# Optimization experiments

Measured on AMD Instinct MI355X. Metric: run time of the kernel, lower is better.

The kernel has to match this reference:

```python
import jax, jax.numpy as jnp
import numpy as np
from jax import lax

BS, T, D = 32, 2048, 256
H, L = 256, 2

def setup_inputs() -> dict:
    key = jax.random.key(0)
    ks = jax.random.split(key, 5)
    s = 1.0 / np.sqrt(H)
    x = jax.random.normal(ks[0], (BS, T, D), dtype=jnp.float32)
    Wx = jax.random.uniform(ks[1], (L, 3 * H, D), jnp.float32, -s, s)
    Wh = jax.random.uniform(ks[2], (L, 3 * H, H), jnp.float32, -s, s)
    bx = jax.random.uniform(ks[3], (L, 3 * H), jnp.float32, -s, s)
    bh = jax.random.uniform(ks[4], (L, 3 * H), jnp.float32, -s, s)
    return {"x": x, "Wx": Wx, "Wh": Wh, "bx": bx, "bh": bh}

def _gru_scan(gx, Wh, bh, h0):
    # gx: (T, bs, L, 3H) precomputed input-side gates; h0: (bs, L, H)
    def step(h, gx_t):
        gh = jnp.einsum('blh,lgh->blg', h, Wh) + bh  # (bs, L, 3H)
        xr, xz, xn = jnp.split(gx_t, 3, axis=-1)
        hr, hz, hn = jnp.split(gh, 3, axis=-1)
        r = jax.nn.sigmoid(xr + hr)
        z = jax.nn.sigmoid(xz + hz)
        n = jnp.tanh(xn + r * hn)
        h_new = (1.0 - z) * n + z * h
        return h_new, h_new
    _, hs = lax.scan(step, h0, gx)  # (T, bs, L, H)
    return hs

def reference(x, Wx, Wh, bx, bh):
    bs, t, _ = x.shape
    l, h = Wh.shape[0], Wh.shape[2]
    # Input-side gate projections for all timesteps/layers at once (each layer
    # consumes the raw input x_t, as in the source module).
    gx = jnp.einsum('btd,lgd->tblg', x, Wx) + bx  # (T, bs, L, 3H)
    h0 = jnp.zeros((bs, l, h), x.dtype)
    fwd = _gru_scan(gx, Wh, bh, h0)               # (T, bs, L, H)
    bwd = _gru_scan(gx[::-1], Wh, bh, h0)[::-1]   # reversed-time pass, same weights
    out = jnp.concatenate([fwd, bwd], axis=-1)    # (T, bs, L, 2H)
    # ordering matches source: for t in range(T): for layer in range(L)
    out = out.transpose(1, 0, 2, 3).reshape(bs, t * l, 2 * h)
    return out
```

## Files before the change

### kernel.cpp

```cpp
#include <hip/hip_runtime.h>


typedef _Float16 half8 __attribute__((ext_vector_type(8)));
typedef _Float16 half2_t __attribute__((ext_vector_type(2)));
typedef float floatx4 __attribute__((ext_vector_type(4)));

__device__ __forceinline__ float sigmoidf_fast(float x) {
    return 1.0f / (1.0f + __expf(-x));
}

__device__ __forceinline__ float tanh_fast(float x) {
    float ax = fabsf(x);
    float e = __expf(-2.0f * ax);
    float t = (1.0f - e) / (1.0f + e);
    return copysignf(t, x);
}

__global__ __launch_bounds__(256) void gemm_gx_kernel(
    const float* __restrict__ x,
    const float* __restrict__ Wx,
    const float* __restrict__ bx,
    _Float16* __restrict__ gx)
{
    __shared__ __align__(16) char lds[32768];
    _Float16* As = (_Float16*)lds;
    _Float16* Bs = (_Float16*)(lds + 8192);

    const int tid = threadIdx.x;
    const int m0 = blockIdx.x * 128;
    const int n0 = blockIdx.y * 128;
    const int wave = tid >> 6;
    const int lane = tid & 63;
    const int wm = wave & 1;
    const int wn = wave >> 1;
    const int frag = lane & 15;
    const int kg = lane >> 4;

    floatx4 acc[4][4];
#pragma unroll
    for (int a = 0; a < 4; ++a)
#pragma unroll
        for (int b = 0; b < 4; ++b)
            acc[a][b] = (floatx4){0.f, 0.f, 0.f, 0.f};

    for (int k0 = 0; k0 < 256; k0 += 32) {
        __syncthreads();
#pragma unroll
        for (int rep = 0; rep < 2; ++rep) {
            int idx = tid + rep * 256;
            int row = idx >> 2;
            int kc = idx & 3;
            const float4* ap = (const float4*)(x + (size_t)(m0 + row) * 256 + k0 + kc * 8);
            const float4* bp = (const float4*)(Wx + (size_t)(n0 + row) * 256 + k0 + kc * 8);
            float4 a0 = ap[0], a1 = ap[1];
            float4 b0 = bp[0], b1 = bp[1];
            half8 av = {(_Float16)a0.x, (_Float16)a0.y, (_Float16)a0.z, (_Float16)a0.w,
                        (_Float16)a1.x, (_Float16)a1.y, (_Float16)a1.z, (_Float16)a1.w};
            half8 bv = {(_Float16)b0.x, (_Float16)b0.y, (_Float16)b0.z, (_Float16)b0.w,
                        (_Float16)b1.x, (_Float16)b1.y, (_Float16)b1.z, (_Float16)b1.w};
            *(half8*)(As + (kc * 128 + row) * 8) = av;
            *(half8*)(Bs + (kc * 128 + row) * 8) = bv;
        }
        __syncthreads();

        half8 af[4], bfr[4];
#pragma unroll
        for (int tm = 0; tm < 4; ++tm)
            af[tm] = *(const half8*)(As + (kg * 128 + wm * 64 + tm * 16 + frag) * 8);
#pragma unroll
        for (int tn = 0; tn < 4; ++tn)
            bfr[tn] = *(const half8*)(Bs + (kg * 128 + wn * 64 + tn * 16 + frag) * 8);
#pragma unroll
        for (int tm = 0; tm < 4; ++tm)
#pragma unroll
            for (int tn = 0; tn < 4; ++tn)
                acc[tm][tn] = __builtin_amdgcn_mfma_f32_16x16x32_f16(
                    af[tm], bfr[tn], acc[tm][tn], 0, 0, 0);
    }

    __syncthreads();
    _Float16* epi = (_Float16*)lds;
#pragma unroll
    for (int tm = 0; tm < 4; ++tm) {
#pragma unroll
        for (int tn = 0; tn < 4; ++tn) {
            int col = wn * 64 + tn * 16 + frag;
            float bias = bx[n0 + col];
#pragma unroll
            for (int r = 0; r < 4; ++r) {
                int rowc = wm * 64 + tm * 16 + kg * 4 + r;
                epi[rowc * 128 + col] = (_Float16)(acc[tm][tn][r] + bias);
            }
        }
    }
    __syncthreads();

    int row = tid >> 1;
    int hs = tid & 1;
    int gm = m0 + row;
    int bb = gm >> 11;
    int tt = gm & 2047;
    int l = n0 / 768;
    int g0 = n0 - l * 768 + hs * 64;
    size_t oidx = (((size_t)bb * 2 + l) * 2048 + tt) * 768 + g0;
    const uint4* s = (const uint4*)(epi + row * 128 + hs * 64);
    uint4* d = (uint4*)(gx + oidx);
#pragma unroll
    for (int j = 0; j < 8; ++j) d[j] = s[j];
}

__global__ __launch_bounds__(512, 1) void gru_scan_kernel(
    const float* __restrict__ Wh,
    const float* __restrict__ bh,
    const _Float16* __restrict__ gx,
    float* __restrict__ out)
{
    const int c = blockIdx.x;
    const int b = c & 31;
    const int l = (c >> 5) & 1;
    const int dir = c >> 6;
    const int tid = threadIdx.x;
    const int i = tid & 255;
    const int q = tid >> 8;

    __shared__ __align__(16) _Float16 h2[256];
    __shared__ float part[3][256];
    __shared__ unsigned int gxb[2][384];

    half2_t wr[64], wz[64], wn_[64];
    {
        const float2* pr = (const float2*)(Wh + ((size_t)l * 768 + i) * 256 + q * 128);
        const float2* pz = (const float2*)(Wh + ((size_t)l * 768 + 256 + i) * 256 + q * 128);
        const float2* pn = (const float2*)(Wh + ((size_t)l * 768 + 512 + i) * 256 + q * 128);
#pragma unroll
        for (int j = 0; j < 64; ++j) {
            float2 a = pr[j], bb2 = pz[j], cc = pn[j];
            wr[j]  = (half2_t){(_Float16)a.x, (_Float16)a.y};
            wz[j]  = (half2_t){(_Float16)bb2.x, (_Float16)bb2.y};
            wn_[j] = (half2_t){(_Float16)cc.x, (_Float16)cc.y};
        }
    }

    const float bhr = bh[l * 768 + i];
    const float bhz = bh[l * 768 + 256 + i];
    const float bhn = bh[l * 768 + 512 + i];

    const unsigned int* gxrow = (const unsigned int*)gx + (size_t)(b * 2 + l) * 2048 * 384;
    float* outp = out + (size_t)b * 2048 * 1024 + (size_t)l * 512 + dir * 256 + i;

    if (tid < 256) h2[tid] = (_Float16)0.f;
    {
        int t0 = dir ? 2047 : 0;
        if (tid < 384) gxb[0][tid] = gxrow[(size_t)t0 * 384 + tid];
    }
    __syncthreads();

    float hreg = 0.f;

    for (int s = 0; s < 2048; ++s) {
        const int t = dir ? (2047 - s) : s;
        const int sn = (s < 2047) ? (s + 1) : s;
        const int tn = dir ? (2047 - sn) : sn;

        unsigned int pf = 0;
        if (tid < 384) pf = gxrow[(size_t)tn * 384 + tid];

        float ar = 0.f, az = 0.f, an = 0.f;
        const half2_t* hp = ((const half2_t*)h2) + q * 64;
#pragma unroll
        for (int j = 0; j < 64; ++j) {
            half2_t hv = hp[j];
            ar = __builtin_amdgcn_fdot2(wr[j], hv, ar, false);
            az = __builtin_amdgcn_fdot2(wz[j], hv, az, false);
            an = __builtin_amdgcn_fdot2(wn_[j], hv, an, false);
        }
        if (q) { part[0][i] = ar; part[1][i] = az; part[2][i] = an; }
        __syncthreads();

        if (tid < 256) {
            float ghr = ar + part[0][i] + bhr;
            float ghz = az + part[1][i] + bhz;
            float ghn = an + part[2][i] + bhn;
            const _Float16* gxc = (const _Float16*)(&gxb[s & 1][0]);
            float xr = (float)gxc[i];
            float xz = (float)gxc[256 + i];
            float xn = (float)gxc[512 + i];
            float r = sigmoidf_fast(xr + ghr);
            float z = sigmoidf_fast(xz + ghz);
            float n = tanh_fast(xn + r * ghn);
            float hnew = (1.f - z) * n + z * hreg;
            hreg = hnew;
            outp[(size_t)t * 1024] = hnew;
            h2[i] = (_Float16)hnew;
        }
        if (tid < 384) gxb[sn & 1][tid] = pf;
        __syncthreads();
    }
}

extern "C" void kernel_launch(void* const* d_in, const int* in_sizes, int n_in,
                              void* d_out, int out_size, void* d_ws, size_t ws_size,
                              hipStream_t stream) {
    const float* x  = (const float*)d_in[0];
    const float* Wx = (const float*)d_in[1];
    const float* Wh = (const float*)d_in[2];
    const float* bx = (const float*)d_in[3];
    const float* bh = (const float*)d_in[4];
    float* out = (float*)d_out;
    _Float16* gxbuf = (_Float16*)d_ws;

    gemm_gx_kernel<<<dim3(512, 12), 256, 0, stream>>>(x, Wx, bx, gxbuf);

    gru_scan_kernel<<<dim3(128), 512, 0, stream>>>(Wh, bh, gxbuf, out);
}
```

Measured before the change: 2.965 ms.

## Reduce GRU scan partial sums within waves via shuffles, double-buffer hidden state

Each output unit now has its two K-halves in the two halves of the same wave, so the partial sums combine with a cross-lane shuffle instead of a shared-memory array. This removes one of the two block barriers per timestep. The hidden state in shared memory is double-buffered, and the input-gate values are prefetched per thread straight from global memory into registers rather than staged through LDS. h is read with 128-bit LDS loads. A dead tanh computation is left in the code and should be optimized away; the waves_per_eu hint may change register allocation for the large register-resident weights.

```diff
diff --git a/kernel.cpp b/kernel.cpp
--- a/kernel.cpp
+++ b/kernel.cpp
@@ -109,7 +109,9 @@
     for (int j = 0; j < 8; ++j) d[j] = s[j];
 }
 
-__global__ __launch_bounds__(512, 1) void gru_scan_kernel(
+__global__ __launch_bounds__(512)
+__attribute__((amdgpu_waves_per_eu(2, 2)))
+void gru_scan_kernel(
     const float* __restrict__ Wh,
     const float* __restrict__ bh,
     const _Float16* __restrict__ gx,
@@ -120,12 +122,12 @@
     const int l = (c >> 5) & 1;
     const int dir = c >> 6;
     const int tid = threadIdx.x;
-    const int i = tid & 255;
-    const int q = tid >> 8;
-
-    __shared__ __align__(16) _Float16 h2[256];
-    __shared__ float part[3][256];
-    __shared__ unsigned int gxb[2][384];
+    const int wave = tid >> 6;
+    const int lane = tid & 63;
+    const int q = lane >> 5;
+    const int i = wave * 32 + (lane & 31);
+
+    __shared__ __align__(16) _Float16 h2[2][256];
 
     half2_t wr[64], wz[64], wn_[64];
     {
@@ -145,14 +147,15 @@
     const float bhz = bh[l * 768 + 256 + i];
     const float bhn = bh[l * 768 + 512 + i];
 
-    const unsigned int* gxrow = (const unsigned int*)gx + (size_t)(b * 2 + l) * 2048 * 384;
+    const _Float16* gxp = gx + (size_t)(b * 2 + l) * 2048 * 768;
     float* outp = out + (size_t)b * 2048 * 1024 + (size_t)l * 512 + dir * 256 + i;
 
-    if (tid < 256) h2[tid] = (_Float16)0.f;
-    {
-        int t0 = dir ? 2047 : 0;
-        if (tid < 384) gxb[0][tid] = gxrow[(size_t)t0 * 384 + tid];
-    }
+    if (tid < 256) h2[0][tid] = (_Float16)0.f;
+
+    const int t0 = dir ? 2047 : 0;
+    _Float16 cxr = gxp[(size_t)t0 * 768 + i];
+    _Float16 cxz = gxp[(size_t)t0 * 768 + 256 + i];
+    _Float16 cxn = gxp[(size_t)t0 * 768 + 512 + i];
     __syncthreads();
 
     float hreg = 0.f;
@@ -162,38 +165,51 @@
         const int sn = (s < 2047) ? (s + 1) : s;
         const int tn = dir ? (2047 - sn) : sn;
 
-        unsigned int pf = 0;
-        if (tid < 384) pf = gxrow[(size_t)tn * 384 + tid];
+        _Float16 pxr = gxp[(size_t)tn * 768 + i];
+        _Float16 pxz = gxp[(size_t)tn * 768 + 256 + i];
+        _Float16 pxn = gxp[(size_t)tn * 768 + 512 + i];
 
         float ar = 0.f, az = 0.f, an = 0.f;
-        const half2_t* hp = ((const half2_t*)h2) + q * 64;
-#pragma unroll
-        for (int j = 0; j < 64; ++j) {
-            half2_t hv = hp[j];
-            ar = __builtin_amdgcn_fdot2(wr[j], hv, ar, false);
-            az = __builtin_amdgcn_fdot2(wz[j], hv, az, false);
-            an = __builtin_amdgcn_fdot2(wn_[j], hv, an, false);
-        }
-        if (q) { part[0][i] = ar; part[1][i] = az; part[2][i] = an; }
-        __syncthreads();
-
-        if (tid < 256) {
-            float ghr = ar + part[0][i] + bhr;
-            float ghz = az + part[1][i] + bhz;
-            float ghn = an + part[2][i] + bhn;
-            const _Float16* gxc = (const _Float16*)(&gxb[s & 1][0]);
-            float xr = (float)gxc[i];
-            float xz = (float)gxc[256 + i];
-            float xn = (float)gxc[512 + i];
-            float r = sigmoidf_fast(xr + ghr);
-            float z = sigmoidf_fast(xz + ghz);
-            float n = tanh_fast(xn + r * ghn);
-            float hnew = (1.f - z) * n + z * hreg;
-            hreg = hnew;
+        const uint4* hbase = (const uint4*)(&h2[s & 1][0]) + (q << 4);
+#pragma unroll
+        for (int j = 0; j < 16; ++j) {
+            uint4 hv = hbase[j];
+            half2_t h0 = __builtin_bit_cast(half2_t, hv.x);
+            half2_t h1 = __builtin_bit_cast(half2_t, hv.y);
+            half2_t hg = __builtin_bit_cast(half2_t, hv.z);
+            half2_t h3 = __builtin_bit_cast(half2_t, hv.w);
+            ar = __builtin_amdgcn_fdot2(wr[4 * j + 0], h0, ar, false);
+            az = __builtin_amdgcn_fdot2(wz[4 * j + 0], h0, az, false);
+            an = __builtin_amdgcn_fdot2(wn_[4 * j + 0], h0, an, false);
+            ar = __builtin_amdgcn_fdot2(wr[4 * j + 1], h1, ar, false);
+            az = __builtin_amdgcn_fdot2(wz[4 * j + 1], h1, az, false);
+            an = __builtin_amdgcn_fdot2(wn_[4 * j + 1], h1, an, false);
+            ar = __builtin_amdgcn_fdot2(wr[4 * j + 2], hg, ar, false);
+            az = __builtin_amdgcn_fdot2(wz[4 * j + 2], hg, az, false);
+            an = __builtin_amdgcn_fdot2(wn_[4 * j + 2], hg, an, false);
+            ar = __builtin_amdgcn_fdot2(wr[4 * j + 3], h3, ar, false);
+            az = __builtin_amdgcn_fdot2(wz[4 * j + 3], h3, az, false);
+            an = __builtin_amdgcn_fdot2(wn_[4 * j + 3], h3, an, false);
+        }
+
+        ar += __shfl_xor(ar, 32, 64);
+        az += __shfl_xor(az, 32, 64);
+        an += __shfl_xor(an, 32, 64);
+
+        float r = sigmoidf_fast((float)cxr + ar + bhr);
+        float z = sigmoidf_fast((float)cxz + az + bhz);
+        float n = tanh_fast((float)cxn + an + r * (an * 0.f + (az * 0.f) + (ar * 0.f) + bhn + an - an + (float)0) + 0.f * an);
+        (void)n;
+        float ghn = an + bhn;
+        n = tanh_fast((float)cxn + r * ghn);
+        float hnew = (1.f - z) * n + z * hreg;
+        hreg = hnew;
+
+        if (q == 0) {
             outp[(size_t)t * 1024] = hnew;
-            h2[i] = (_Float16)hnew;
-        }
-        if (tid < 384) gxb[sn & 1][tid] = pf;
+            h2[(s + 1) & 1][i] = (_Float16)hnew;
+        }
+        cxr = pxr; cxz = pxz; cxn = pxn;
         __syncthreads();
     }
 }
```

Result: faster. 2.881 ms (-2.9%).
